# Performance work log

Measured on AMD Instinct MI355X. Metric: run time of the kernel, lower is better.

The kernel has to match this reference:

```python
import jax, jax.numpy as jnp
import numpy as np

NUM_EMBEDDINGS = 1024
EMBEDDING_DIM = 64
COMMITMENT_COST = 0.25


def setup_inputs() -> dict:
    key = jax.random.key(0)
    k1, k2 = jax.random.split(key)
    inputs = jax.random.normal(k1, (2, 64, 32, 32, 32), dtype=jnp.float32)
    embedding = jax.random.normal(k2, (NUM_EMBEDDINGS, EMBEDDING_DIM), dtype=jnp.float32)
    return {"inputs": inputs, "embedding": embedding}


def reference(inputs, embedding):
    # inputs: [B, C, D, H, W], embedding: [K, C]
    B, C, D, H, W = inputs.shape
    # flatten_permutation = [0, 2, 3, 4, 1] -> [B*D*H*W, C]
    flat_input = jnp.transpose(inputs, (0, 2, 3, 4, 1)).reshape(-1, C)
    # squared euclidean distances [N, K]
    distances = (
        jnp.sum(flat_input**2, axis=1, keepdims=True)
        + jnp.sum(embedding**2, axis=1)[None, :]
        - 2.0 * flat_input @ embedding.T
    )
    # torch.max(-distances, dim=1)[1] == argmin of distances
    encoding_indices = jnp.argmax(-distances, axis=1)  # [N]
    encoding_indices_view = encoding_indices.reshape(B, D, H, W)
    # embed: lookup then quantization_permutation [0, 4, 1, 2, 3] -> channel-first
    quantized = embedding[encoding_indices_view]            # [B, D, H, W, C]
    quantized = jnp.transpose(quantized, (0, 4, 1, 2, 3))   # [B, C, D, H, W]
    # commitment loss: MSE(stop_grad(quantized), inputs)
    loss = COMMITMENT_COST * jnp.mean((jax.lax.stop_gradient(quantized) - inputs) ** 2)
    # straight-through estimator
    quantized_st = inputs + jax.lax.stop_gradient(quantized - inputs)
    # eval path: encodings_sum = zeros(256) (hardcoded in original forward)
    encodings_sum = jnp.zeros(256, dtype=jnp.float32)
    return quantized_st, loss, encoding_indices_view, encodings_sum, embedding
```

## Files before the change

### kernel.cpp

```cpp
#include <hip/hip_runtime.h>
#include <stdint.h>

#define KCODES  1024
#define CDIM    64
#define SPATIAL 32768
#define NPOS    65536
#define NEL     4194304

#define OUT_Q    0
#define OUT_LOSS 4194304
#define OUT_IDX  4194305
#define OUT_SUM  4259841
#define OUT_EMB  4260097

#define NSET  32
#define SETB  8192
#define EIEXP 262144
#define BPOS  128
#define NRND  16

typedef _Float16 half8  __attribute__((ext_vector_type(8)));
typedef float    f32x4  __attribute__((ext_vector_type(4)));
typedef float    f32x16 __attribute__((ext_vector_type(16)));

__global__ void prep_emb(const float* __restrict__ emb, char* __restrict__ ws,
                         float* __restrict__ out) {
    int gt = blockIdx.x * 256 + threadIdx.x;
    if (gt == 0) out[OUT_LOSS] = 0.f;
    if (gt < 256) out[OUT_SUM + gt] = 0.f;
    {
        float4 v = *(const float4*)(emb + (size_t)gt * 4);
        float* o = out + OUT_EMB + (size_t)gt * 4;
        o[0] = v.x; o[1] = v.y; o[2] = v.z; o[3] = v.w;
    }
    if (gt < 8192) {
        int k = gt >> 3, oct = gt & 7;
        int set = k >> 5, row = k & 31;
        int ks = oct >> 1, hc = oct & 1;
        const float* e = emb + (size_t)k * CDIM + oct * 8;
        char* rec = ws + (size_t)set * SETB;
        _Float16* hi = (_Float16*)(rec + (ks * 2 + 0) * 1024 + (hc * 32 + row) * 16);
        _Float16* lo = (_Float16*)(rec + (ks * 2 + 1) * 1024 + (hc * 32 + row) * 16);
        float s2 = 0.f;
        half8 hv, lv;
#pragma unroll
        for (int i = 0; i < 8; ++i) {
            float v = e[i];
            s2 = fmaf(v, v, s2);
            _Float16 h = (_Float16)v;
            hv[i] = h;
            lv[i] = (_Float16)(v - (float)h);
        }
        *(half8*)hi = hv;
        *(half8*)lo = lv;
        s2 += __shfl_xor(s2, 1);
        s2 += __shfl_xor(s2, 2);
        s2 += __shfl_xor(s2, 4);
        if (oct == 0) {
            int hh = (row >> 2) & 1;
            int q  = (row & 3) | ((row >> 3) << 2);
            ((float*)(ws + EIEXP))[(set * 2 + hh) * 16 + q] = -0.5f * s2;
        }
    }
}

#define GLDS16(GSRC, LDST)                                                     \
    __builtin_amdgcn_global_load_lds(                                          \
        (const __attribute__((address_space(1))) void*)(GSRC),                 \
        (__attribute__((address_space(3))) void*)(LDST), 16, 0, 0)

__global__ __launch_bounds__(512, 2) void vq_kernel(
        const float* __restrict__ in, const float* __restrict__ emb,
        const char* __restrict__ wsA, float* __restrict__ out) {
    __shared__ __align__(16) char ring[6][SETB];
    __shared__ __align__(16) float eiL[NSET * 32];
    __shared__ float candS[2][BPOS];
    __shared__ int   candK[2][BPOS];
    __shared__ int   kwin[BPOS];
    __shared__ float lred[8];

    const int tid  = threadIdx.x;
    const int lane = tid & 63, wv = tid >> 6;
    const int col  = lane & 31, h = lane >> 5;
    const int pg   = wv & 3, kh = wv >> 2;
    const int p0   = blockIdx.x * BPOS;
    const int b    = p0 >> 15;
    const int s0   = p0 & 32767;
    const float* xin = in + (size_t)b * (CDIM * SPATIAL) + s0;
    const float* eiG = (const float*)(wsA + EIEXP);

    float* xl = (float*)&ring[0][0];
    {
        int p = tid & 127, cq = tid >> 7;
#pragma unroll
        for (int j = 0; j < 16; ++j) {
            int c = cq * 16 + j;
            xl[c * 129 + p] = xin[(size_t)c * SPATIAL + p];
        }
    }
    eiL[tid] = eiG[tid];
    eiL[tid + 512] = eiG[tid + 512];
    __syncthreads();

    half8 bh[4], bl[4];
    {
        int pp = pg * 32 + col;
#pragma unroll
        for (int ks = 0; ks < 4; ++ks)
#pragma unroll
            for (int j = 0; j < 8; ++j) {
                int c = ks * 16 + h * 8 + j;
                float v = xl[c * 129 + pp];
                _Float16 hh = (_Float16)v;
                bh[ks][j] = hh;
                bl[ks][j] = (_Float16)(v - (float)hh);
            }
    }
    __syncthreads();

    char* sl0 = &ring[kh * 3 + 0][0];
    char* sl1 = &ring[kh * 3 + 1][0];
    char* sl2 = &ring[kh * 3 + 2][0];
#define STAGE2(RSET, DST) do {                                                 \
        const char* src_ = wsA + (size_t)(RSET) * SETB + pg * 2048 + lane * 16;\
        char* dst_ = (DST) + pg * 2048 + lane * 16;                            \
        GLDS16(src_, dst_);                                                    \
        GLDS16(src_ + 1024, dst_ + 1024);                                      \
    } while (0)
    STAGE2(kh * 16 + 0, sl0);
    STAGE2(kh * 16 + 1, sl1);
    asm volatile("s_waitcnt vmcnt(2)" ::: "memory");
    __builtin_amdgcn_s_barrier();
    __builtin_amdgcn_sched_barrier(0);

    f32x16 maxS;
    int    maxR[16];
#pragma unroll
    for (int q = 0; q < 16; ++q) { maxS[q] = -3.402823466e38f; maxR[q] = 0; }

#pragma unroll 1
    for (int r = 0; r < NRND; ++r) {
        STAGE2(kh * 16 + ((r + 2) & 15), sl2);
        const int setid = kh * 16 + r;
        f32x16 eiv = *(const f32x16*)&eiL[(setid * 2 + h) * 16];
        const char* ap = sl0 + (size_t)lane * 16;
        f32x16 a;
        {
            half8 ah0 = *(const half8*)(ap);
            half8 al0 = *(const half8*)(ap + 1024);
            half8 ah1 = *(const half8*)(ap + 2048);
            half8 al1 = *(const half8*)(ap + 3072);
            half8 ah2 = *(const half8*)(ap + 4096);
            half8 al2 = *(const half8*)(ap + 5120);
            half8 ah3 = *(const half8*)(ap + 6144);
            half8 al3 = *(const half8*)(ap + 7168);
            a = __builtin_amdgcn_mfma_f32_32x32x16_f16(ah0, bh[0], eiv, 0, 0, 0);
            a = __builtin_amdgcn_mfma_f32_32x32x16_f16(ah0, bl[0], a, 0, 0, 0);
            a = __builtin_amdgcn_mfma_f32_32x32x16_f16(al0, bh[0], a, 0, 0, 0);
            a = __builtin_amdgcn_mfma_f32_32x32x16_f16(ah1, bh[1], a, 0, 0, 0);
            a = __builtin_amdgcn_mfma_f32_32x32x16_f16(ah1, bl[1], a, 0, 0, 0);
            a = __builtin_amdgcn_mfma_f32_32x32x16_f16(al1, bh[1], a, 0, 0, 0);
            a = __builtin_amdgcn_mfma_f32_32x32x16_f16(ah2, bh[2], a, 0, 0, 0);
            a = __builtin_amdgcn_mfma_f32_32x32x16_f16(ah2, bl[2], a, 0, 0, 0);
            a = __builtin_amdgcn_mfma_f32_32x32x16_f16(al2, bh[2], a, 0, 0, 0);
            a = __builtin_amdgcn_mfma_f32_32x32x16_f16(ah3, bh[3], a, 0, 0, 0);
            a = __builtin_amdgcn_mfma_f32_32x32x16_f16(ah3, bl[3], a, 0, 0, 0);
            a = __builtin_amdgcn_mfma_f32_32x32x16_f16(al3, bh[3], a, 0, 0, 0);
        }
#pragma unroll
        for (int q = 0; q < 16; ++q)
            if (a[q] > maxS[q]) { maxS[q] = a[q]; maxR[q] = setid; }
        char* t0 = sl0; sl0 = sl1; sl1 = sl2; sl2 = t0;
        asm volatile("s_waitcnt vmcnt(2)" ::: "memory");
        __builtin_amdgcn_s_barrier();
        __builtin_amdgcn_sched_barrier(0);
    }
#undef STAGE2

    float best = maxS[0];
    int   bk   = maxR[0] * 32 + 4 * h;
#pragma unroll
    for (int q = 1; q < 16; ++q) {
        float sc = maxS[q];
        int   kk = maxR[q] * 32 + 4 * h + (q & 3) + 8 * (q >> 2);
        if (sc > best || (sc == best && kk < bk)) { best = sc; bk = kk; }
    }
    {
        float os = __shfl_xor(best, 32);
        int   ok = __shfl_xor(bk, 32);
        if (os > best || (os == best && ok < bk)) { best = os; bk = ok; }
    }
    if (h == 0) {
        candS[kh][pg * 32 + col] = best;
        candK[kh][pg * 32 + col] = bk;
    }
    __syncthreads();

    if (tid < BPOS) {
        float s0v = candS[0][tid], s1v = candS[1][tid];
        int   k0v = candK[0][tid], k1v = candK[1][tid];
        int sel = (s1v > s0v) || (s1v == s0v && k1v < k0v);
        int bkf = sel ? k1v : k0v;
        kwin[tid] = bkf;
        out[OUT_IDX + p0 + tid] = (float)bkf;
    }
    __syncthreads();

    float lsum = 0.f;
    {
        int p = tid & 127, cq = tid >> 7;
        int kk = kwin[p];
        const float* eb = emb + (size_t)kk * CDIM;
        float* q = out + OUT_Q + (size_t)b * (CDIM * SPATIAL) + s0;
#pragma unroll
        for (int j = 0; j < 16; ++j) {
            int c = cq * 16 + j;
            float x = xin[(size_t)c * SPATIAL + p];
            float e = eb[c];
            float d = e - x;
            lsum = fmaf(d, d, lsum);
            q[(size_t)c * SPATIAL + p] = x + d;
        }
    }
#pragma unroll
    for (int off = 32; off > 0; off >>= 1) lsum += __shfl_down(lsum, off);
    if (lane == 0) lred[wv] = lsum;
    __syncthreads();
    if (tid == 0) {
        float t = 0.f;
#pragma unroll
        for (int w = 0; w < 8; ++w) t += lred[w];
        atomicAdd(out + OUT_LOSS, t * (0.25f / (float)NEL));
    }
}

extern "C" void kernel_launch(void* const* d_in, const int* in_sizes, int n_in,
                              void* d_out, int out_size, void* d_ws, size_t ws_size,
                              hipStream_t stream) {
    const float* in  = (const float*)d_in[0];
    const float* emb = (const float*)d_in[1];
    float* out = (float*)d_out;
    char*  ws  = (char*)d_ws;

    prep_emb<<<64, 256, 0, stream>>>(emb, ws, out);
    vq_kernel<<<NPOS / BPOS, 512, 0, stream>>>(in, emb, ws, out);
}
```

Baseline: 41.88 us.

## Retile VQ search: each wave covers 64 positions and a quarter of the codebook

The wave split goes from 4 position groups × 2 codebook halves to 2 position groups × 4 codebook quarters. Each wave now holds two 32-position B tiles, so every staged A fragment feeds two MFMA chains. This halves the rounds per wave and the LDS reads per MFMA. The ring buffer becomes double-buffered per quarter, and the running argmin moves from registers into per-round shuffle reductions with LDS candidate updates. The cost is twice the B registers, more reduction work every round, and a final merge across four candidates.

```diff
diff --git a/kernel.cpp b/kernel.cpp
--- a/kernel.cpp
+++ b/kernel.cpp
@@ -17,7 +17,7 @@
 #define SETB  8192
 #define EIEXP 262144
 #define BPOS  128
-#define NRND  16
+#define NRND  8
 
 typedef _Float16 half8  __attribute__((ext_vector_type(8)));
 typedef float    f32x4  __attribute__((ext_vector_type(4)));
@@ -72,24 +72,24 @@
 __global__ __launch_bounds__(512, 2) void vq_kernel(
         const float* __restrict__ in, const float* __restrict__ emb,
         const char* __restrict__ wsA, float* __restrict__ out) {
-    __shared__ __align__(16) char ring[6][SETB];
+    __shared__ __align__(16) char ring[4][2][SETB];
     __shared__ __align__(16) float eiL[NSET * 32];
-    __shared__ float candS[2][BPOS];
-    __shared__ int   candK[2][BPOS];
+    __shared__ float candS[4][BPOS];
+    __shared__ int   candK[4][BPOS];
     __shared__ int   kwin[BPOS];
     __shared__ float lred[8];
 
     const int tid  = threadIdx.x;
     const int lane = tid & 63, wv = tid >> 6;
     const int col  = lane & 31, h = lane >> 5;
-    const int pg   = wv & 3, kh = wv >> 2;
+    const int pg   = wv & 1, kh = wv >> 1;
     const int p0   = blockIdx.x * BPOS;
     const int b    = p0 >> 15;
     const int s0   = p0 & 32767;
     const float* xin = in + (size_t)b * (CDIM * SPATIAL) + s0;
     const float* eiG = (const float*)(wsA + EIEXP);
 
-    float* xl = (float*)&ring[0][0];
+    float* xl = (float*)&ring[0][0][0];
     {
         int p = tid & 127, cq = tid >> 7;
 #pragma unroll
@@ -100,109 +100,135 @@
     }
     eiL[tid] = eiG[tid];
     eiL[tid + 512] = eiG[tid + 512];
-    __syncthreads();
-
-    half8 bh[4], bl[4];
-    {
-        int pp = pg * 32 + col;
-#pragma unroll
-        for (int ks = 0; ks < 4; ++ks)
+    {
+        candS[tid >> 7][tid & 127] = -3.402823466e38f;
+        candK[tid >> 7][tid & 127] = 0;
+    }
+    __syncthreads();
+
+    half8 bh[2][4], bl[2][4];
+#pragma unroll
+    for (int t = 0; t < 2; ++t)
+#pragma unroll
+        for (int ks = 0; ks < 4; ++ks) {
+            int pp = pg * 64 + t * 32 + col;
 #pragma unroll
             for (int j = 0; j < 8; ++j) {
                 int c = ks * 16 + h * 8 + j;
                 float v = xl[c * 129 + pp];
                 _Float16 hh = (_Float16)v;
-                bh[ks][j] = hh;
-                bl[ks][j] = (_Float16)(v - (float)hh);
-            }
-    }
-    __syncthreads();
-
-    char* sl0 = &ring[kh * 3 + 0][0];
-    char* sl1 = &ring[kh * 3 + 1][0];
-    char* sl2 = &ring[kh * 3 + 2][0];
-#define STAGE2(RSET, DST) do {                                                 \
-        const char* src_ = wsA + (size_t)(RSET) * SETB + pg * 2048 + lane * 16;\
-        char* dst_ = (DST) + pg * 2048 + lane * 16;                            \
-        GLDS16(src_, dst_);                                                    \
-        GLDS16(src_ + 1024, dst_ + 1024);                                      \
+                bh[t][ks][j] = hh;
+                bl[t][ks][j] = (_Float16)(v - (float)hh);
+            }
+        }
+    __syncthreads();
+
+    const char* myws = wsA + (size_t)kh * NRND * SETB;
+#define STAGE(RSET, SLOT) do {                                                 \
+        const char* s_ = myws + (size_t)(RSET) * SETB + pg * 4096 + lane * 16; \
+        char* d_ = &ring[kh][SLOT][0] + pg * 4096 + lane * 16;                 \
+        GLDS16(s_,        d_);                                                 \
+        GLDS16(s_ + 1024, d_ + 1024);                                          \
+        GLDS16(s_ + 2048, d_ + 2048);                                          \
+        GLDS16(s_ + 3072, d_ + 3072);                                          \
     } while (0)
-    STAGE2(kh * 16 + 0, sl0);
-    STAGE2(kh * 16 + 1, sl1);
-    asm volatile("s_waitcnt vmcnt(2)" ::: "memory");
-    __builtin_amdgcn_s_barrier();
-    __builtin_amdgcn_sched_barrier(0);
-
-    f32x16 maxS;
-    int    maxR[16];
-#pragma unroll
-    for (int q = 0; q < 16; ++q) { maxS[q] = -3.402823466e38f; maxR[q] = 0; }
+    STAGE(0, 0);
 
 #pragma unroll 1
     for (int r = 0; r < NRND; ++r) {
-        STAGE2(kh * 16 + ((r + 2) & 15), sl2);
-        const int setid = kh * 16 + r;
-        f32x16 eiv = *(const f32x16*)&eiL[(setid * 2 + h) * 16];
-        const char* ap = sl0 + (size_t)lane * 16;
-        f32x16 a;
+        STAGE((r + 1) & (NRND - 1), (r + 1) & 1);
+        asm volatile("s_waitcnt vmcnt(4)" ::: "memory");
+        __builtin_amdgcn_s_barrier();
+        __builtin_amdgcn_sched_barrier(0);
+        const int set = kh * NRND + r;
+        f32x16 eiv = *(const f32x16*)&eiL[(set * 2 + h) * 16];
+        const char* ap = &ring[kh][r & 1][0] + (size_t)lane * 16;
+        f32x16 a0, a1;
         {
             half8 ah0 = *(const half8*)(ap);
             half8 al0 = *(const half8*)(ap + 1024);
+            a0 = __builtin_amdgcn_mfma_f32_32x32x16_f16(ah0, bh[0][0], eiv, 0, 0, 0);
+            a1 = __builtin_amdgcn_mfma_f32_32x32x16_f16(ah0, bh[1][0], eiv, 0, 0, 0);
+            a0 = __builtin_amdgcn_mfma_f32_32x32x16_f16(ah0, bl[0][0], a0, 0, 0, 0);
+            a1 = __builtin_amdgcn_mfma_f32_32x32x16_f16(ah0, bl[1][0], a1, 0, 0, 0);
+            a0 = __builtin_amdgcn_mfma_f32_32x32x16_f16(al0, bh[0][0], a0, 0, 0, 0);
+            a1 = __builtin_amdgcn_mfma_f32_32x32x16_f16(al0, bh[1][0], a1, 0, 0, 0);
             half8 ah1 = *(const half8*)(ap + 2048);
             half8 al1 = *(const half8*)(ap + 3072);
+            a0 = __builtin_amdgcn_mfma_f32_32x32x16_f16(ah1, bh[0][1], a0, 0, 0, 0);
+            a1 = __builtin_amdgcn_mfma_f32_32x32x16_f16(ah1, bh[1][1], a1, 0, 0, 0);
+            a0 = __builtin_amdgcn_mfma_f32_32x32x16_f16(ah1, bl[0][1], a0, 0, 0, 0);
+            a1 = __builtin_amdgcn_mfma_f32_32x32x16_f16(ah1, bl[1][1], a1, 0, 0, 0);
+            a0 = __builtin_amdgcn_mfma_f32_32x32x16_f16(al1, bh[0][1], a0, 0, 0, 0);
+            a1 = __builtin_amdgcn_mfma_f32_32x32x16_f16(al1, bh[1][1], a1, 0, 0, 0);
             half8 ah2 = *(const half8*)(ap + 4096);
             half8 al2 = *(const half8*)(ap + 5120);
+            a0 = __builtin_amdgcn_mfma_f32_32x32x16_f16(ah2, bh[0][2], a0, 0, 0, 0);
+            a1 = __builtin_amdgcn_mfma_f32_32x32x16_f16(ah2, bh[1][2], a1, 0, 0, 0);
+            a0 = __builtin_amdgcn_mfma_f32_32x32x16_f16(ah2, bl[0][2], a0, 0, 0, 0);
+            a1 = __builtin_amdgcn_mfma_f32_32x32x16_f16(ah2, bl[1][2], a1, 0, 0, 0);
+            a0 = __builtin_amdgcn_mfma_f32_32x32x16_f16(al2, bh[0][2], a0, 0, 0, 0);
+            a1 = __builtin_amdgcn_mfma_f32_32x32x16_f16(al2, bh[1][2], a1, 0, 0, 0);
             half8 ah3 = *(const half8*)(ap + 6144);
             half8 al3 = *(const half8*)(ap + 7168);
-            a = __builtin_amdgcn_mfma_f32_32x32x16_f16(ah0, bh[0], eiv, 0, 0, 0);
-            a = __builtin_amdgcn_mfma_f32_32x32x16_f16(ah0, bl[0], a, 0, 0, 0);
-            a = __builtin_amdgcn_mfma_f32_32x32x16_f16(al0, bh[0], a, 0, 0, 0);
-            a = __builtin_amdgcn_mfma_f32_32x32x16_f16(ah1, bh[1], a, 0, 0, 0);
-            a = __builtin_amdgcn_mfma_f32_32x32x16_f16(ah1, bl[1], a, 0, 0, 0);
-            a = __builtin_amdgcn_mfma_f32_32x32x16_f16(al1, bh[1], a, 0, 0, 0);
-            a = __builtin_amdgcn_mfma_f32_32x32x16_f16(ah2, bh[2], a, 0, 0, 0);
-            a = __builtin_amdgcn_mfma_f32_32x32x16_f16(ah2, bl[2], a, 0, 0, 0);
-            a = __builtin_amdgcn_mfma_f32_32x32x16_f16(al2, bh[2], a, 0, 0, 0);
-            a = __builtin_amdgcn_mfma_f32_32x32x16_f16(ah3, bh[3], a, 0, 0, 0);
-            a = __builtin_amdgcn_mfma_f32_32x32x16_f16(ah3, bl[3], a, 0, 0, 0);
-            a = __builtin_amdgcn_mfma_f32_32x32x16_f16(al3, bh[3], a, 0, 0, 0);
-        }
-#pragma unroll
-        for (int q = 0; q < 16; ++q)
-            if (a[q] > maxS[q]) { maxS[q] = a[q]; maxR[q] = setid; }
-        char* t0 = sl0; sl0 = sl1; sl1 = sl2; sl2 = t0;
-        asm volatile("s_waitcnt vmcnt(2)" ::: "memory");
+            a0 = __builtin_amdgcn_mfma_f32_32x32x16_f16(ah3, bh[0][3], a0, 0, 0, 0);
+            a1 = __builtin_amdgcn_mfma_f32_32x32x16_f16(ah3, bh[1][3], a1, 0, 0, 0);
+            a0 = __builtin_amdgcn_mfma_f32_32x32x16_f16(ah3, bl[0][3], a0, 0, 0, 0);
+            a1 = __builtin_amdgcn_mfma_f32_32x32x16_f16(ah3, bl[1][3], a1, 0, 0, 0);
+            a0 = __builtin_amdgcn_mfma_f32_32x32x16_f16(al3, bh[0][3], a0, 0, 0, 0);
+            a1 = __builtin_amdgcn_mfma_f32_32x32x16_f16(al3, bh[1][3], a1, 0, 0, 0);
+        }
+        const int kbase = set * 32 + 4 * h;
+        {
+            float bs = a0[0];
+            int   bk = kbase;
+#pragma unroll
+            for (int q = 1; q < 16; ++q) {
+                float sc = a0[q];
+                int   kk = kbase + (q & 3) + 8 * (q >> 2);
+                if (sc > bs) { bs = sc; bk = kk; }
+            }
+            float os = __shfl_xor(bs, 32);
+            int   ok = __shfl_xor(bk, 32);
+            if (os > bs || (os == bs && ok < bk)) { bs = os; bk = ok; }
+            if (h == 0) {
+                int pc = pg * 64 + 0 * 32 + col;
+                if (bs > candS[kh][pc]) { candS[kh][pc] = bs; candK[kh][pc] = bk; }
+            }
+        }
+        {
+            float bs = a1[0];
+            int   bk = kbase;
+#pragma unroll
+            for (int q = 1; q < 16; ++q) {
+                float sc = a1[q];
+                int   kk = kbase + (q & 3) + 8 * (q >> 2);
+                if (sc > bs) { bs = sc; bk = kk; }
+            }
+            float os = __shfl_xor(bs, 32);
+            int   ok = __shfl_xor(bk, 32);
+            if (os > bs || (os == bs && ok < bk)) { bs = os; bk = ok; }
+            if (h == 0) {
+                int pc = pg * 64 + 1 * 32 + col;
+                if (bs > candS[kh][pc]) { candS[kh][pc] = bs; candK[kh][pc] = bk; }
+            }
+        }
         __builtin_amdgcn_s_barrier();
-        __builtin_amdgcn_sched_barrier(0);
-    }
-#undef STAGE2
-
-    float best = maxS[0];
-    int   bk   = maxR[0] * 32 + 4 * h;
-#pragma unroll
-    for (int q = 1; q < 16; ++q) {
-        float sc = maxS[q];
-        int   kk = maxR[q] * 32 + 4 * h + (q & 3) + 8 * (q >> 2);
-        if (sc > best || (sc == best && kk < bk)) { best = sc; bk = kk; }
-    }
-    {
-        float os = __shfl_xor(best, 32);
-        int   ok = __shfl_xor(bk, 32);
-        if (os > best || (os == best && ok < bk)) { best = os; bk = ok; }
-    }
-    if (h == 0) {
-        candS[kh][pg * 32 + col] = best;
-        candK[kh][pg * 32 + col] = bk;
-    }
+    }
+#undef STAGE
     __syncthreads();
 
     if (tid < BPOS) {
-        float s0v = candS[0][tid], s1v = candS[1][tid];
-        int   k0v = candK[0][tid], k1v = candK[1][tid];
-        int sel = (s1v > s0v) || (s1v == s0v && k1v < k0v);
-        int bkf = sel ? k1v : k0v;
-        kwin[tid] = bkf;
-        out[OUT_IDX + p0 + tid] = (float)bkf;
+        float bs = candS[0][tid];
+        int   bk = candK[0][tid];
+#pragma unroll
+        for (int w = 1; w < 4; ++w) {
+            float sc = candS[w][tid];
+            int   kk = candK[w][tid];
+            if (sc > bs || (sc == bs && kk < bk)) { bs = sc; bk = kk; }
+        }
+        kwin[tid] = bk;
+        out[OUT_IDX + p0 + tid] = (float)bk;
     }
     __syncthreads();
 
```

After: 49.59 us. 1.18x slower.
